# Kernel tuning notes

Hardware: AMD Instinct MI355X
Metric: run time of the kernel (lower is better)

## Reference

```python
import jax, jax.numpy as jnp
import numpy as np

HID = 64

def _rnn_layer(x, W_ih, W_hh, b_ih, b_hh):
    # x: [B, T, F]; PyTorch RNN step: h_t = tanh(x_t @ W_ih.T + b_ih + h_{t-1} @ W_hh.T + b_hh)
    # Precompute the input projection for all timesteps as one big GEMM.
    x_proj = jnp.einsum('btf,hf->bth', x, W_ih) + b_ih  # [B, T, H]
    B = x.shape[0]
    h0 = jnp.zeros((B, HID), x.dtype)

    def step(h, xt):
        h = jnp.tanh(xt + h @ W_hh.T + b_hh)
        return h, h

    _, hs = jax.lax.scan(step, h0, jnp.swapaxes(x_proj, 0, 1))  # hs: [T, B, H]
    return jnp.swapaxes(hs, 0, 1)  # [B, T, H]


def setup_inputs() -> dict:
    key = jax.random.key(0)
    ks = jax.random.split(key, 20)
    B, T, F = 4096, 128, 14
    s_in = 1.0 / np.sqrt(HID)  # PyTorch RNN init scale
    d = {
        'x': jax.random.normal(ks[0], (B, T, F), jnp.float32),
        'W_ih0': jax.random.normal(ks[1], (HID, F), jnp.float32) * s_in,
        'W_hh0': jax.random.normal(ks[2], (HID, HID), jnp.float32) * s_in,
        'b_ih0': jax.random.normal(ks[3], (HID,), jnp.float32) * s_in,
        'b_hh0': jax.random.normal(ks[4], (HID,), jnp.float32) * s_in,
        'W_ih1': jax.random.normal(ks[5], (HID, HID), jnp.float32) * s_in,
        'W_hh1': jax.random.normal(ks[6], (HID, HID), jnp.float32) * s_in,
        'b_ih1': jax.random.normal(ks[7], (HID,), jnp.float32) * s_in,
        'b_hh1': jax.random.normal(ks[8], (HID,), jnp.float32) * s_in,
        'W_ih2': jax.random.normal(ks[9], (HID, HID), jnp.float32) * s_in,
        'W_hh2': jax.random.normal(ks[10], (HID, HID), jnp.float32) * s_in,
        'b_ih2': jax.random.normal(ks[11], (HID,), jnp.float32) * s_in,
        'b_hh2': jax.random.normal(ks[12], (HID,), jnp.float32) * s_in,
        'fc1_w': jax.random.normal(ks[13], (32, HID), jnp.float32) * s_in,
        'fc1_b': jax.random.normal(ks[14], (32,), jnp.float32) * s_in,
        'fc2_w': jax.random.normal(ks[15], (1, 32), jnp.float32) * (1.0 / np.sqrt(32)),
        'fc2_b': jax.random.normal(ks[16], (1,), jnp.float32) * (1.0 / np.sqrt(32)),
    }
    return d


def reference(x, W_ih0, W_hh0, b_ih0, b_hh0, W_ih1, W_hh1, b_ih1, b_hh1,
              W_ih2, W_hh2, b_ih2, b_hh2, fc1_w, fc1_b, fc2_w, fc2_b):
    h = _rnn_layer(x, W_ih0, W_hh0, b_ih0, b_hh0)
    h = _rnn_layer(h, W_ih1, W_hh1, b_ih1, b_hh1)
    h = _rnn_layer(h, W_ih2, W_hh2, b_ih2, b_hh2)
    last = h[:, -1, :]                       # [B, H]
    y = jax.nn.relu(last @ fc1_w.T + fc1_b)  # [B, 32]
    return y @ fc2_w.T + fc2_b               # [B, 1]
```

## Files before the change

### kernel.cpp

```cpp
#include <hip/hip_runtime.h>

typedef short  s16x8 __attribute__((ext_vector_type(8)));
typedef float  f32x4 __attribute__((ext_vector_type(4)));
typedef float  f32x2 __attribute__((ext_vector_type(2)));
typedef unsigned int u32;
typedef unsigned int u32x4 __attribute__((ext_vector_type(4)));
typedef unsigned short u16;

#define DEVI static __device__ __forceinline__

#if __has_builtin(__builtin_amdgcn_exp2f)
#define EXP2(v) __builtin_amdgcn_exp2f(v)
#else
#define EXP2(v) exp2f(v)
#endif

constexpr int T_  = 128;
constexpr int F_  = 14;
constexpr int H_  = 64;
constexpr int BPB = 16;
constexpr int K_  = 8;
constexpr int NCH = T_ / K_;

DEVI u16 f2bf(float f) {
  u32 u = __builtin_bit_cast(u32, f);
  u += 0x7fffu + ((u >> 16) & 1u);
  return (u16)(u >> 16);
}
DEVI u32 cvtpk(float a, float b) {
  u32 r;
  asm("v_cvt_pk_bf16_f32 %0, %1, %2" : "=v"(r) : "v"(a), "v"(b));
  return r;
}
DEVI s16x8 packfrag(const f32x4& a, const f32x4& b) {
  u32x4 p;
  p[0] = cvtpk(a[0], a[1]); p[1] = cvtpk(a[2], a[3]);
  p[2] = cvtpk(b[0], b[1]); p[3] = cvtpk(b[2], b[3]);
  return __builtin_bit_cast(s16x8, p);
}
DEVI f32x4 tanh4(const f32x4& v) {
  const f32x4 kC = -2.8853900817779268f;
  f32x4 t = v * kC;
  f32x4 e;
  e[0] = EXP2(t[0]); e[1] = EXP2(t[1]);
  e[2] = EXP2(t[2]); e[3] = EXP2(t[3]);
  const f32x4 kOne = 1.0f;
  f32x4 d = e + kOne;
  f32x4 r;
  r[0] = __builtin_amdgcn_rcpf(d[0]); r[1] = __builtin_amdgcn_rcpf(d[1]);
  r[2] = __builtin_amdgcn_rcpf(d[2]); r[3] = __builtin_amdgcn_rcpf(d[3]);
  const f32x4 kTwo = 2.0f, kNegOne = -1.0f;
  return __builtin_elementwise_fma(kTwo, r, kNegOne);
}
DEVI f32x4 MFMA(s16x8 a, s16x8 b, f32x4 c) {
  return __builtin_amdgcn_mfma_f32_16x16x32_bf16(a, b, c, 0, 0, 0);
}
DEVI s16x8 ldrow8(const float* p) {
  const f32x4 a = ((const f32x4*)p)[0];
  const f32x4 b = ((const f32x4*)p)[1];
  s16x8 r;
  r[0] = (short)f2bf(a[0]); r[1] = (short)f2bf(a[1]);
  r[2] = (short)f2bf(a[2]); r[3] = (short)f2bf(a[3]);
  r[4] = (short)f2bf(b[0]); r[5] = (short)f2bf(b[1]);
  r[6] = (short)f2bf(b[2]); r[7] = (short)f2bf(b[3]);
  return r;
}

__global__ __launch_bounds__(192, 1) void rnn_ck(
    const float* __restrict__ x,
    const float* __restrict__ Wih0, const float* __restrict__ Whh0,
    const float* __restrict__ bih0, const float* __restrict__ bhh0,
    const float* __restrict__ Wih1, const float* __restrict__ Whh1,
    const float* __restrict__ bih1, const float* __restrict__ bhh1,
    const float* __restrict__ Wih2, const float* __restrict__ Whh2,
    const float* __restrict__ bih2, const float* __restrict__ bhh2,
    const float* __restrict__ fc1w, const float* __restrict__ fc1b,
    const float* __restrict__ fc2w, const float* __restrict__ fc2b,
    float* __restrict__ out)
{
  __shared__ __align__(16) u32x4 hf[2][2][K_][2][64];

  const int tid  = threadIdx.x;
  const int w    = tid >> 6;
  const int lane = tid & 63;
  const int g    = lane >> 4;
  const int m    = lane & 15;
  const int b0   = blockIdx.x * BPB;

  f32x4 z4; z4[0] = 0.f; z4[1] = 0.f; z4[2] = 0.f; z4[3] = 0.f;

  s16x8 Ax[4], Ai[4][2], Ah[4][2];
  f32x4 bc[4];
  {
    const float* Wi = Wih1; const float* Wh = Whh0;
    const float* bi = bih0; const float* bh = bhh0;
    if (w == 1)      { Wi = Wih1; Wh = Whh1; bi = bih1; bh = bhh1; }
    else if (w == 2) { Wi = Wih2; Wh = Whh2; bi = bih2; bh = bhh2; }
    #pragma unroll
    for (int n = 0; n < 4; n++) {
      const int Lr = 32 * (n & 1) + 8 * (m >> 2) + 4 * (n >> 1) + (m & 3);
      if (w == 0) {
        s16x8 r;
        #pragma unroll
        for (int j2 = 0; j2 < 8; j2++) {
          const int kk = 8 * g + j2;
          r[j2] = (kk < F_) ? (short)f2bf(Wih0[Lr * F_ + kk]) : (short)0;
        }
        Ax[n] = r;
        Ai[n][0] = r; Ai[n][1] = r;
      } else {
        #pragma unroll
        for (int kt = 0; kt < 2; kt++)
          Ai[n][kt] = ldrow8(Wi + Lr * H_ + 32 * kt + 8 * g);
        Ax[n] = Ai[n][0];
      }
      #pragma unroll
      for (int kt = 0; kt < 2; kt++)
        Ah[n][kt] = ldrow8(Wh + Lr * H_ + 32 * kt + 8 * g);
      const int Lb = 32 * (n & 1) + 8 * g + 4 * (n >> 1);
      bc[n] = *(const f32x4*)(bi + Lb) + *(const f32x4*)(bh + Lb);
    }
  }

  s16x8 F[2];
  {
    s16x8 z;
    #pragma unroll
    for (int i = 0; i < 8; i++) z[i] = 0;
    F[0] = z; F[1] = z;
  }
  f32x4 h2v[4];
  #pragma unroll
  for (int n = 0; n < 4; n++) h2v[n] = z4;

  const float* xrow = x + (size_t)(b0 + m) * T_ * F_;
  auto ldraw = [&](int t, f32x4& ra, f32x4& rb) {
    const float* p = xrow + t * F_;
    if (g == 0) {
      f32x2 p0 = *(const f32x2*)(p),     p1 = *(const f32x2*)(p + 2);
      f32x2 p2 = *(const f32x2*)(p + 4), p3 = *(const f32x2*)(p + 6);
      ra[0] = p0[0]; ra[1] = p0[1]; ra[2] = p1[0]; ra[3] = p1[1];
      rb[0] = p2[0]; rb[1] = p2[1]; rb[2] = p3[0]; rb[3] = p3[1];
    } else if (g == 1) {
      f32x2 p4 = *(const f32x2*)(p + 8), p5 = *(const f32x2*)(p + 10);
      f32x2 p6 = *(const f32x2*)(p + 12);
      ra[0] = p4[0]; ra[1] = p4[1]; ra[2] = p5[0]; ra[3] = p5[1];
      rb[0] = p6[0]; rb[1] = p6[1]; rb[2] = 0.f;   rb[3] = 0.f;
    } else {
      ra = z4; rb = z4;
    }
  };
  auto cvtraw = [&](const f32x4& ra, const f32x4& rb) -> s16x8 {
    u32x4 p;
    p[0] = cvtpk(ra[0], ra[1]); p[1] = cvtpk(ra[2], ra[3]);
    p[2] = cvtpk(rb[0], rb[1]); p[3] = cvtpk(rb[2], rb[3]);
    return __builtin_bit_cast(s16x8, p);
  };

  s16x8 cur[K_];
  {
    f32x4 ira[K_], irb[K_];
    if (w == 0) {
      #pragma unroll
      for (int k = 0; k < K_; k++) { ldraw(k, ira[k], irb[k]); }
      #pragma unroll
      for (int k = 0; k < K_; k++) cur[k] = cvtraw(ira[k], irb[k]);
    }
  }

  #pragma unroll 1
  for (int e = 0; e < NCH + 2; e++) {
    const int c    = e - w;
    const int wb   = e & 1, rbuf = (e & 1) ^ 1;

    f32x4 stage[2 * K_];

    if (w == 0) {
      int cn = e + 1; if (cn > NCH - 1) cn = NCH - 1;
      #pragma unroll
      for (int k = 0; k < K_; k++) ldraw(cn * K_ + k, stage[k], stage[K_ + k]);
    }

    if (c >= 0 && c < NCH) {
      if (w > 0) {
        const int src = w - 1;
        #pragma unroll
        for (int k = 0; k < K_; k++) {
          stage[k]      = __builtin_bit_cast(f32x4, hf[rbuf][src][k][0][lane]);
          stage[K_ + k] = __builtin_bit_cast(f32x4, hf[rbuf][src][k][1][lane]);
        }
      }

      f32x4 qc[4], qn[4];
      if (w == 0) {
        #pragma unroll
        for (int n = 0; n < 4; n++) qc[n] = MFMA(Ax[n], cur[0], z4);
      } else {
        const s16x8 P0 = __builtin_bit_cast(s16x8, stage[0]);
        const s16x8 P1 = __builtin_bit_cast(s16x8, stage[K_]);
        #pragma unroll
        for (int n = 0; n < 4; n++) qc[n] = MFMA(Ai[n][0], P0, z4);
        #pragma unroll
        for (int n = 0; n < 4; n++) qc[n] = MFMA(Ai[n][1], P1, qc[n]);
      }

      #pragma unroll
      for (int k = 0; k < K_; k++) {
        if (k + 1 < K_) {
          if (w == 0) {
            #pragma unroll
            for (int n = 0; n < 4; n++) qn[n] = MFMA(Ax[n], cur[k + 1], z4);
          } else {
            const s16x8 P0 = __builtin_bit_cast(s16x8, stage[k + 1]);
            const s16x8 P1 = __builtin_bit_cast(s16x8, stage[K_ + k + 1]);
            #pragma unroll
            for (int n = 0; n < 4; n++) qn[n] = MFMA(Ai[n][0], P0, z4);
            #pragma unroll
            for (int n = 0; n < 4; n++) qn[n] = MFMA(Ai[n][1], P1, qn[n]);
          }
        }

        f32x4 p[4];
        p[0] = MFMA(Ah[0][0], F[0], bc[0]);
        p[2] = MFMA(Ah[2][0], F[0], bc[2]);
        p[1] = MFMA(Ah[1][0], F[0], bc[1]);
        p[3] = MFMA(Ah[3][0], F[0], bc[3]);
        p[0] = MFMA(Ah[0][1], F[1], p[0]);
        p[2] = MFMA(Ah[2][1], F[1], p[2]);
        p[1] = MFMA(Ah[1][1], F[1], p[1]);
        p[3] = MFMA(Ah[3][1], F[1], p[3]);

        f32x4 hv0 = tanh4(p[0] + qc[0]);
        f32x4 hv2 = tanh4(p[2] + qc[2]);
        F[0] = packfrag(hv0, hv2);
        f32x4 hv1 = tanh4(p[1] + qc[1]);
        f32x4 hv3 = tanh4(p[3] + qc[3]);
        F[1] = packfrag(hv1, hv3);

        if (w < 2) {
          hf[wb][w][k][0][lane] = __builtin_bit_cast(u32x4, F[0]);
          hf[wb][w][k][1][lane] = __builtin_bit_cast(u32x4, F[1]);
        } else if (c == NCH - 1 && k == K_ - 1) {
          h2v[0] = hv0; h2v[1] = hv1;
          h2v[2] = hv2; h2v[3] = hv3;
        }

        if (k + 1 < K_) {
          #pragma unroll
          for (int n = 0; n < 4; n++) qc[n] = qn[n];
        }

        if (w == 0 && k >= 2)
          cur[k - 2] = cvtraw(stage[k - 2], stage[K_ + k - 2]);
      }

      if (w == 0) {
        cur[K_ - 2] = cvtraw(stage[K_ - 2], stage[2 * K_ - 2]);
        cur[K_ - 1] = cvtraw(stage[K_ - 1], stage[2 * K_ - 1]);
      }
    }
    __syncthreads();
  }

  float (*h2l)[68] = (float (*)[68])&hf[0][0][0][0][0];
  if (w == 2) {
    #pragma unroll
    for (int n = 0; n < 4; n++) {
      const int Lb = 32 * (n & 1) + 8 * g + 4 * (n >> 1);
      *(f32x4*)&h2l[m][Lb] = h2v[n];
    }
  }
  __syncthreads();

  if (w == 0) {
    float hr[64];
    #pragma unroll
    for (int q = 0; q < 16; q++) {
      f32x4 v = *(const f32x4*)&h2l[m][4 * q];
      hr[4 * q + 0] = v[0]; hr[4 * q + 1] = v[1];
      hr[4 * q + 2] = v[2]; hr[4 * q + 3] = v[3];
    }
    float acc2 = 0.f;
    #pragma unroll
    for (int jj = 0; jj < 8; jj++) {
      const int jf = 8 * g + jj;
      float s = fc1b[jf];
      const f32x4* wp = (const f32x4*)(fc1w + jf * H_);
      #pragma unroll
      for (int kq = 0; kq < 16; kq++) {
        f32x4 wv = wp[kq];
        s += hr[4 * kq + 0] * wv[0] + hr[4 * kq + 1] * wv[1]
           + hr[4 * kq + 2] * wv[2] + hr[4 * kq + 3] * wv[3];
      }
      s = fmaxf(s, 0.f);
      acc2 += s * fc2w[jf];
    }
    acc2 += __shfl_xor(acc2, 16, 64);
    acc2 += __shfl_xor(acc2, 32, 64);
    if (lane < 16) out[b0 + m] = acc2 + fc2b[0];
  }
}

extern "C" void kernel_launch(void* const* d_in, const int* in_sizes, int n_in,
                              void* d_out, int out_size, void* d_ws, size_t ws_size,
                              hipStream_t stream) {
  const float* x    = (const float*)d_in[0];
  const float* Wih0 = (const float*)d_in[1];
  const float* Whh0 = (const float*)d_in[2];
  const float* bih0 = (const float*)d_in[3];
  const float* bhh0 = (const float*)d_in[4];
  const float* Wih1 = (const float*)d_in[5];
  const float* Whh1 = (const float*)d_in[6];
  const float* bih1 = (const float*)d_in[7];
  const float* bhh1 = (const float*)d_in[8];
  const float* Wih2 = (const float*)d_in[9];
  const float* Whh2 = (const float*)d_in[10];
  const float* bih2 = (const float*)d_in[11];
  const float* bhh2 = (const float*)d_in[12];
  const float* fc1w = (const float*)d_in[13];
  const float* fc1b = (const float*)d_in[14];
  const float* fc2w = (const float*)d_in[15];
  const float* fc2b = (const float*)d_in[16];

  rnn_ck<<<dim3(4096 / BPB), dim3(192), 0, stream>>>(
      x, Wih0, Whh0, bih0, bhh0, Wih1, Whh1, bih1, bhh1,
      Wih2, Whh2, bih2, bhh2, fc1w, fc1b, fc2w, fc2b, (float*)d_out);
}
```

Measured before the change: 179.7 us.

## Add dedicated loader wave to prefetch x chunks into shared memory

Adds a fourth wavefront that loads the next chunk of x from global memory, converts it to bf16 and writes it to a double-buffered shared-memory area, so the layer-0 wave no longer issues global loads or conversions inside its recurrence. The bias is now folded into the input-projection MFMA accumulator, which removes a vector add before each tanh. This is meant to take load latency and conversion work off the critical serial path. In exchange each block has more threads and a larger dynamic shared-memory footprint, and layer 0 adds shared-memory reads per chunk.

New measurement: 167.5 us. -6.8%, faster.

```diff
diff --git a/kernel.cpp b/kernel.cpp
--- a/kernel.cpp
+++ b/kernel.cpp
@@ -21,6 +21,10 @@
 constexpr int BPB = 16;
 constexpr int K_  = 8;
 constexpr int NCH = T_ / K_;
+
+constexpr int HF_BYTES   = 2 * 2 * K_ * 2 * 64 * 16;
+constexpr int XBUF_BYTES = 2 * K_ * 64 * 16;
+constexpr int SMEM_BYTES = HF_BYTES + XBUF_BYTES;
 
 DEVI u16 f2bf(float f) {
   u32 u = __builtin_bit_cast(u32, f);
@@ -66,7 +70,7 @@
   return r;
 }
 
-__global__ __launch_bounds__(192, 1) void rnn_ck(
+__global__ __launch_bounds__(256, 1) void rnn_ck(
     const float* __restrict__ x,
     const float* __restrict__ Wih0, const float* __restrict__ Whh0,
     const float* __restrict__ bih0, const float* __restrict__ bhh0,
@@ -78,7 +82,9 @@
     const float* __restrict__ fc2w, const float* __restrict__ fc2b,
     float* __restrict__ out)
 {
-  __shared__ __align__(16) u32x4 hf[2][2][K_][2][64];
+  extern __shared__ __align__(16) char smem[];
+  u32x4 (*hf)[2][K_][2][64] = (u32x4 (*)[2][K_][2][64])smem;
+  u32x4 (*xbuf)[K_][64]     = (u32x4 (*)[K_][64])(smem + HF_BYTES);
 
   const int tid  = threadIdx.x;
   const int w    = tid >> 6;
@@ -91,7 +97,7 @@
 
   s16x8 Ax[4], Ai[4][2], Ah[4][2];
   f32x4 bc[4];
-  {
+  if (w < 3) {
     const float* Wi = Wih1; const float* Wh = Whh0;
     const float* bi = bih0; const float* bh = bhh0;
     if (w == 1)      { Wi = Wih1; Wh = Whh1; bi = bih1; bh = bhh1; }
@@ -157,112 +163,112 @@
     return __builtin_bit_cast(s16x8, p);
   };
 
-  s16x8 cur[K_];
-  {
-    f32x4 ira[K_], irb[K_];
-    if (w == 0) {
-      #pragma unroll
-      for (int k = 0; k < K_; k++) { ldraw(k, ira[k], irb[k]); }
-      #pragma unroll
-      for (int k = 0; k < K_; k++) cur[k] = cvtraw(ira[k], irb[k]);
-    }
-  }
+  if (w == 3) {
+    f32x4 ra[K_], rb[K_];
+    #pragma unroll
+    for (int k = 0; k < K_; k++) ldraw(k, ra[k], rb[k]);
+    #pragma unroll
+    for (int k = 0; k < K_; k++)
+      xbuf[0][k][lane] = __builtin_bit_cast(u32x4, cvtraw(ra[k], rb[k]));
+  }
+  __syncthreads();
 
   #pragma unroll 1
   for (int e = 0; e < NCH + 2; e++) {
-    const int c    = e - w;
-    const int wb   = e & 1, rbuf = (e & 1) ^ 1;
-
-    f32x4 stage[2 * K_];
-
-    if (w == 0) {
-      int cn = e + 1; if (cn > NCH - 1) cn = NCH - 1;
-      #pragma unroll
-      for (int k = 0; k < K_; k++) ldraw(cn * K_ + k, stage[k], stage[K_ + k]);
-    }
-
-    if (c >= 0 && c < NCH) {
-      if (w > 0) {
-        const int src = w - 1;
+    const int wb = e & 1, rbuf = wb ^ 1;
+
+    if (w == 3) {
+      if (e < NCH - 1) {
+        f32x4 ra[K_], rb[K_];
+        #pragma unroll
+        for (int k = 0; k < K_; k++) ldraw((e + 1) * K_ + k, ra[k], rb[k]);
+        #pragma unroll
+        for (int k = 0; k < K_; k++)
+          xbuf[rbuf][k][lane] = __builtin_bit_cast(u32x4, cvtraw(ra[k], rb[k]));
+      }
+    } else {
+      const int c = e - w;
+      if (c >= 0 && c < NCH) {
+        s16x8 cur[K_];
+        f32x4 stage[2 * K_];
+        if (w == 0) {
+          #pragma unroll
+          for (int k = 0; k < K_; k++)
+            cur[k] = __builtin_bit_cast(s16x8, xbuf[wb][k][lane]);
+        } else {
+          const int src = w - 1;
+          #pragma unroll
+          for (int k = 0; k < K_; k++) {
+            stage[k]      = __builtin_bit_cast(f32x4, hf[rbuf][src][k][0][lane]);
+            stage[K_ + k] = __builtin_bit_cast(f32x4, hf[rbuf][src][k][1][lane]);
+          }
+        }
+
+        f32x4 qc[4], qn[4];
+        if (w == 0) {
+          #pragma unroll
+          for (int n = 0; n < 4; n++) qc[n] = MFMA(Ax[n], cur[0], bc[n]);
+        } else {
+          const s16x8 P0 = __builtin_bit_cast(s16x8, stage[0]);
+          const s16x8 P1 = __builtin_bit_cast(s16x8, stage[K_]);
+          #pragma unroll
+          for (int n = 0; n < 4; n++) qc[n] = MFMA(Ai[n][0], P0, bc[n]);
+          #pragma unroll
+          for (int n = 0; n < 4; n++) qc[n] = MFMA(Ai[n][1], P1, qc[n]);
+        }
+
         #pragma unroll
         for (int k = 0; k < K_; k++) {
-          stage[k]      = __builtin_bit_cast(f32x4, hf[rbuf][src][k][0][lane]);
-          stage[K_ + k] = __builtin_bit_cast(f32x4, hf[rbuf][src][k][1][lane]);
+          f32x4 p[4];
+          p[0] = MFMA(Ah[0][0], F[0], qc[0]);
+          p[2] = MFMA(Ah[2][0], F[0], qc[2]);
+          p[1] = MFMA(Ah[1][0], F[0], qc[1]);
+          p[3] = MFMA(Ah[3][0], F[0], qc[3]);
+          p[0] = MFMA(Ah[0][1], F[1], p[0]);
+          p[2] = MFMA(Ah[2][1], F[1], p[2]);
+          p[1] = MFMA(Ah[1][1], F[1], p[1]);
+          p[3] = MFMA(Ah[3][1], F[1], p[3]);
+
+          if (k + 1 < K_) {
+            if (w == 0) {
+              #pragma unroll
+              for (int n = 0; n < 4; n++) qn[n] = MFMA(Ax[n], cur[k + 1], bc[n]);
+            } else {
+              const s16x8 P0 = __builtin_bit_cast(s16x8, stage[k + 1]);
+              const s16x8 P1 = __builtin_bit_cast(s16x8, stage[K_ + k + 1]);
+              #pragma unroll
+              for (int n = 0; n < 4; n++) qn[n] = MFMA(Ai[n][0], P0, bc[n]);
+              #pragma unroll
+              for (int n = 0; n < 4; n++) qn[n] = MFMA(Ai[n][1], P1, qn[n]);
+            }
+          }
+
+          f32x4 hv0 = tanh4(p[0]);
+          f32x4 hv2 = tanh4(p[2]);
+          F[0] = packfrag(hv0, hv2);
+          f32x4 hv1 = tanh4(p[1]);
+          f32x4 hv3 = tanh4(p[3]);
+          F[1] = packfrag(hv1, hv3);
+
+          if (w < 2) {
+            hf[wb][w][k][0][lane] = __builtin_bit_cast(u32x4, F[0]);
+            hf[wb][w][k][1][lane] = __builtin_bit_cast(u32x4, F[1]);
+          } else if (c == NCH - 1 && k == K_ - 1) {
+            h2v[0] = hv0; h2v[1] = hv1;
+            h2v[2] = hv2; h2v[3] = hv3;
+          }
+
+          if (k + 1 < K_) {
+            #pragma unroll
+            for (int n = 0; n < 4; n++) qc[n] = qn[n];
+          }
         }
       }
-
-      f32x4 qc[4], qn[4];
-      if (w == 0) {
-        #pragma unroll
-        for (int n = 0; n < 4; n++) qc[n] = MFMA(Ax[n], cur[0], z4);
-      } else {
-        const s16x8 P0 = __builtin_bit_cast(s16x8, stage[0]);
-        const s16x8 P1 = __builtin_bit_cast(s16x8, stage[K_]);
-        #pragma unroll
-        for (int n = 0; n < 4; n++) qc[n] = MFMA(Ai[n][0], P0, z4);
-        #pragma unroll
-        for (int n = 0; n < 4; n++) qc[n] = MFMA(Ai[n][1], P1, qc[n]);
-      }
-
-      #pragma unroll
-      for (int k = 0; k < K_; k++) {
-        if (k + 1 < K_) {
-          if (w == 0) {
-            #pragma unroll
-            for (int n = 0; n < 4; n++) qn[n] = MFMA(Ax[n], cur[k + 1], z4);
-          } else {
-            const s16x8 P0 = __builtin_bit_cast(s16x8, stage[k + 1]);
-            const s16x8 P1 = __builtin_bit_cast(s16x8, stage[K_ + k + 1]);
-            #pragma unroll
-            for (int n = 0; n < 4; n++) qn[n] = MFMA(Ai[n][0], P0, z4);
-            #pragma unroll
-            for (int n = 0; n < 4; n++) qn[n] = MFMA(Ai[n][1], P1, qn[n]);
-          }
-        }
-
-        f32x4 p[4];
-        p[0] = MFMA(Ah[0][0], F[0], bc[0]);
-        p[2] = MFMA(Ah[2][0], F[0], bc[2]);
-        p[1] = MFMA(Ah[1][0], F[0], bc[1]);
-        p[3] = MFMA(Ah[3][0], F[0], bc[3]);
-        p[0] = MFMA(Ah[0][1], F[1], p[0]);
-        p[2] = MFMA(Ah[2][1], F[1], p[2]);
-        p[1] = MFMA(Ah[1][1], F[1], p[1]);
-        p[3] = MFMA(Ah[3][1], F[1], p[3]);
-
-        f32x4 hv0 = tanh4(p[0] + qc[0]);
-        f32x4 hv2 = tanh4(p[2] + qc[2]);
-        F[0] = packfrag(hv0, hv2);
-        f32x4 hv1 = tanh4(p[1] + qc[1]);
-        f32x4 hv3 = tanh4(p[3] + qc[3]);
-        F[1] = packfrag(hv1, hv3);
-
-        if (w < 2) {
-          hf[wb][w][k][0][lane] = __builtin_bit_cast(u32x4, F[0]);
-          hf[wb][w][k][1][lane] = __builtin_bit_cast(u32x4, F[1]);
-        } else if (c == NCH - 1 && k == K_ - 1) {
-          h2v[0] = hv0; h2v[1] = hv1;
-          h2v[2] = hv2; h2v[3] = hv3;
-        }
-
-        if (k + 1 < K_) {
-          #pragma unroll
-          for (int n = 0; n < 4; n++) qc[n] = qn[n];
-        }
-
-        if (w == 0 && k >= 2)
-          cur[k - 2] = cvtraw(stage[k - 2], stage[K_ + k - 2]);
-      }
-
-      if (w == 0) {
-        cur[K_ - 2] = cvtraw(stage[K_ - 2], stage[2 * K_ - 2]);
-        cur[K_ - 1] = cvtraw(stage[K_ - 1], stage[2 * K_ - 1]);
-      }
     }
     __syncthreads();
   }
 
-  float (*h2l)[68] = (float (*)[68])&hf[0][0][0][0][0];
+  float (*h2l)[68] = (float (*)[68])smem;
   if (w == 2) {
     #pragma unroll
     for (int n = 0; n < 4; n++) {
@@ -322,7 +328,15 @@
   const float* fc2w = (const float*)d_in[15];
   const float* fc2b = (const float*)d_in[16];
 
-  rnn_ck<<<dim3(4096 / BPB), dim3(192), 0, stream>>>(
+  static bool s_attr_set = false;
+  if (!s_attr_set) {
+    (void)hipFuncSetAttribute((const void*)rnn_ck,
+                              hipFuncAttributeMaxDynamicSharedMemorySize,
+                              SMEM_BYTES);
+    s_attr_set = true;
+  }
+
+  rnn_ck<<<dim3(4096 / BPB), dim3(256), SMEM_BYTES, stream>>>(
       x, Wih0, Whh0, bih0, bhh0, Wih1, Whh1, bih1, bhh1,
       Wih2, Whh2, bih2, bhh2, fc1w, fc1b, fc2w, fc2b, (float*)d_out);
 }
```
